# Performance work log

Hardware: AMD Instinct MI355X
Metric: run time of the kernel (lower is better)

## Reference

```python
import jax, jax.numpy as jnp
import numpy as np

N, E, NG = 8192, 65536, 8
EMB, SH = 32, 9
HID = EMB * SH
SDIM, M, KV = 16, 2048, 16  # M = master_rate*N masters (static top-k); KV virtual nbrs/node
RMAX, NB, PC = 10.0, 8, 5
MLPD, MSH, NL = 64, 32, 3
NEMB = 10


def _radial(r):
    # r: [E,1] -> Bessel basis * polynomial cutoff envelope, [E, NB]
    x = r / RMAX
    n = jnp.arange(1, NB + 1, dtype=r.dtype)
    bes = jnp.sqrt(2.0 / RMAX) * jnp.sin(n * jnp.pi * x) / jnp.maximum(r, 1e-9)
    p = float(PC)
    env = (1.0 - (p + 1) * (p + 2) / 2 * x ** PC + p * (p + 2) * x ** (PC + 1)
           - p * (p + 1) / 2 * x ** (PC + 2))
    env = jnp.where(x < 1.0, env, 0.0)
    return bes * env


def _sph(vec):
    # component-normalized real spherical harmonics l=0,1,2 of normalized vec
    r = jnp.linalg.norm(vec, axis=-1, keepdims=True)
    u = vec / jnp.maximum(r, 1e-9)
    x, y, z = u[..., 0], u[..., 1], u[..., 2]
    s3, s5, s15 = jnp.sqrt(3.0), jnp.sqrt(5.0), jnp.sqrt(15.0)
    Y = jnp.stack([
        jnp.ones_like(x),
        s3 * y, s3 * z, s3 * x,
        s15 * x * y, s15 * y * z, 0.5 * s5 * (3 * z * z - 1.0),
        s15 * x * z, 0.5 * s15 * (x * x - y * y)], axis=-1)
    return Y, r


def _conv(h, src, dst, sh, ef, W, rw1, rb1, rw2, rb2, valid, nnodes):
    # TFN-style conv: per-edge radial MLP -> per-sh-path weights, tensor product, scatter-sum
    rad = jax.nn.relu(ef @ rw1 + rb1) @ rw2 + rb2  # [E, SH]
    coeff = sh * rad                               # [E, SH]
    h_src = h[src]                                 # gather [E, in]
    out = W.shape[-1]
    msg = jnp.zeros((src.shape[0], out), h.dtype)
    for s in range(SH):  # small fixed loop over sh paths (avoids [E,in*SH] blowup)
        msg = msg + coeff[:, s:s + 1] * (h_src @ W[:, s, :])
    if valid is not None:
        msg = msg * valid[:, None]
    return jnp.zeros((nnodes, out), h.dtype).at[dst].add(msg)


def _scatter_softmax(sc, idx, nseg):
    mx = jax.ops.segment_max(sc, idx, nseg)
    e = jnp.exp(sc - mx[idx])
    s = jax.ops.segment_sum(e, idx, nseg)
    return e / (s[idx] + 1e-9)


def _forward(atoms, pos, edge_index, batch_ids, emb_table, W0, W12,
             rw1, rb1, rw2, rb2, msw1, msb1, msw2, msb2,
             vq, vk, aw1, ab1, aw2, ab2, pw1, pb1, pw2, pb2):
    h = emb_table[atoms]
    src, dst = edge_index[0], edge_index[1]
    for i in range(NL):
        W = W0 if i == 0 else W12[i - 1]
        # ---- local message passing over original edges ----
        vec = pos[src] - pos[dst]
        sh, r = _sph(vec)
        ef = _radial(r)
        h_up = _conv(h, src, dst, sh, ef, W, rw1[i], rb1[i], rw2[i], rb2[i], None, N)
        h_local = h_up.at[:, :h.shape[-1]].add(h)  # h_update + right-pad(h)
        # ---- master selection (static top-k of soft scores, k = master_rate*N) ----
        hs = h_local[:, :SDIM]
        m = jax.nn.sigmoid((jax.nn.relu(hs @ msw1[i] + msb1[i]) @ msw2[i] + msb2[i])[:, 0])
        _, midx = jax.lax.top_k(m, M)
        midx = jnp.sort(midx)
        inv = jnp.full((N,), -1, jnp.int32).at[midx].set(jnp.arange(M, dtype=jnp.int32))
        ms, md = inv[src], inv[dst]
        vi = (ms >= 0) & (md >= 0)           # induced-subgraph edge mask
        msc = jnp.where(vi, ms, 0)
        mdc = jnp.where(vi, md, 0)
        vif = vi.astype(h.dtype)
        h_m = h_local[midx]
        pos_m = pos[midx]
        hms = h_m[:, :SDIM]
        # induced dense adjacency over masters
        adj = jnp.minimum(jnp.zeros((M, M), h.dtype).at[msc, mdc].add(vif), 1.0)
        # ---- virtual edge generation (attention over masters) ----
        S = (hms @ vq[i]) @ (hms @ vk[i]).T / jnp.sqrt(jnp.asarray(SDIM, h.dtype))
        blocked = jnp.eye(M, dtype=bool) | (adj > 0)
        S = jnp.where(blocked, -jnp.inf, S)
        A_virtual = jax.nn.softmax(S, axis=-1)
        _, tk = jax.lax.top_k(S, KV)          # top-KV virtual nbrs per master (static)
        row = jnp.repeat(jnp.arange(M), KV)
        col = tk.reshape(-1)
        sv = jnp.concatenate([row, col])      # undirected virtual edges
        dv = jnp.concatenate([col, row])
        # ---- master-level edges: induced (masked) + virtual ----
        srcm = jnp.concatenate([msc, sv])
        dstm = jnp.concatenate([mdc, dv])
        vecm = pos_m[srcm] - pos_m[dstm]
        shm, rm = _sph(vecm)
        efm = _radial(rm)
        # scatter-softmax attention weights on virtual edges
        att_in = jnp.concatenate([hms[sv], hms[dv], efm[E:]], axis=-1)
        sc = (jax.nn.relu(att_in @ aw1[i] + ab1[i]) @ aw2[i] + ab2[i])[:, 0]
        wv = _scatter_softmax(sc, dv, M)
        full_w = jnp.concatenate([vif, wv])   # induced edges weight 1 (0 if invalid)
        efm = efm * full_w[:, None]
        if i == 0:
            h_hier = h_m  # first layer: in_irreps != out_irreps -> skip master conv
        else:
            validm = jnp.concatenate([vif, jnp.ones_like(wv)])
            h_mu = _conv(h_m, srcm, dstm, shm, efm, W,
                         rw1[i], rb1[i], rw2[i], rb2[i], validm, M)
            h_hier = h_mu + h_m
        # ---- scatter masters back, soft mix ----
        h_exp = jnp.zeros_like(h_local).at[midx].set(h_hier)
        me = m[:, None]
        h = (1.0 - me) * h_local + me * h_exp
    pooled = jax.ops.segment_sum(h[:, :EMB], batch_ids, NG)  # global_add_pool
    return jax.nn.relu(pooled @ pw1 + pb1) @ pw2 + pb2


def setup_inputs() -> dict:
    key = jax.random.key(0)
    ks = jax.random.split(key, 30)
    g = lambda k, shape, s=0.1: jax.random.normal(k, shape, jnp.float32) * s
    return dict(
        atoms=jax.random.randint(ks[0], (N,), 0, NEMB),
        pos=jax.random.normal(ks[1], (N, 3), jnp.float32) * 3.0,
        edge_index=jax.random.randint(ks[2], (2, E), 0, N),
        batch_ids=jnp.sort(jax.random.randint(ks[3], (N,), 0, NG)),
        emb_table=g(ks[4], (NEMB, EMB), 1.0),
        W0=g(ks[5], (EMB, SH, HID)),
        W12=g(ks[6], (NL - 1, HID, SH, HID), 0.05),
        rw1=g(ks[7], (NL, NB, MLPD), 0.3), rb1=g(ks[8], (NL, MLPD)),
        rw2=g(ks[9], (NL, MLPD, SH), 0.3), rb2=g(ks[10], (NL, SH)),
        msw1=g(ks[11], (NL, SDIM, MSH), 0.3), msb1=g(ks[12], (NL, MSH)),
        msw2=g(ks[13], (NL, MSH, 1), 0.3), msb2=g(ks[14], (NL, 1)),
        vq=g(ks[15], (NL, SDIM, SDIM), 0.3), vk=g(ks[16], (NL, SDIM, SDIM), 0.3),
        aw1=g(ks[17], (NL, 2 * SDIM + NB, SDIM), 0.3), ab1=g(ks[18], (NL, SDIM)),
        aw2=g(ks[19], (NL, SDIM, 1), 0.3), ab2=g(ks[20], (NL, 1)),
        pw1=g(ks[21], (EMB, EMB), 0.3), pb1=g(ks[22], (EMB,)),
        pw2=g(ks[23], (EMB, 1), 0.3), pb2=g(ks[24], (1,)),
    )


def reference(atoms, pos, edge_index, batch_ids, emb_table, W0, W12,
              rw1, rb1, rw2, rb2, msw1, msb1, msw2, msb2,
              vq, vk, aw1, ab1, aw2, ab2, pw1, pb1, pw2, pb2):
    return _forward(atoms, pos, edge_index, batch_ids, emb_table, W0, W12,
                    rw1, rb1, rw2, rb2, msw1, msb1, msw2, msb2,
                    vq, vk, aw1, ab1, aw2, ab2, pw1, pb1, pw2, pb2)
```

## Files before the change

### kernel.cpp

```cpp
#include <hip/hip_runtime.h>
#include <math.h>

#define NN     8192
#define EE     65536
#define NGR    8
#define EMBD   32
#define NSH    9
#define HIDD   288
#define SD     16
#define MM     2048
#define KVK    16
#define NBAS   8
#define MLPDIM 64
#define MSHD   32
#define MK     (MM*KVK)
#define EH     (EE + 2*MK)

static __device__ __forceinline__ float relu_(float x) { return fmaxf(x, 0.f); }

__device__ __forceinline__ void radial8(float r, float ef[8]) {
  float x = r * 0.1f;
  float invr = 1.0f / fmaxf(r, 1e-9f);
  float env = 0.0f;
  if (x < 1.0f) {
    float x2 = x * x, x4 = x2 * x2, x5 = x4 * x;
    env = 1.0f - 21.0f * x5 + 35.0f * x5 * x - 15.0f * x5 * x2;
  }
  const float cst = 0.4472135954999579f;
  float a = 3.14159265358979323846f * x;
#pragma unroll
  for (int n = 1; n <= NBAS; ++n)
    ef[n - 1] = cst * sinf((float)n * a) * invr * env;
}

__device__ __forceinline__ void sph9(float vx, float vy, float vz, float Y[9], float& r) {
  r = sqrtf(vx * vx + vy * vy + vz * vz);
  float inv = 1.0f / fmaxf(r, 1e-9f);
  float x = vx * inv, y = vy * inv, z = vz * inv;
  const float s3 = 1.7320508075688772f, s5 = 2.23606797749979f, s15 = 3.872983346207417f;
  Y[0] = 1.0f;
  Y[1] = s3 * y; Y[2] = s3 * z; Y[3] = s3 * x;
  Y[4] = s15 * x * y; Y[5] = s15 * y * z;
  Y[6] = 0.5f * s5 * (3.0f * z * z - 1.0f);
  Y[7] = s15 * x * z;
  Y[8] = 0.5f * s15 * (x * x - y * y);
}

__device__ __forceinline__ void radmlp(const float ef[8], const float* w1, const float* b1,
                                       const float* w2, const float* b2, float rad[9]) {
  float z[MLPDIM];
#pragma unroll
  for (int d = 0; d < MLPDIM; ++d) {
    float a = b1[d];
#pragma unroll
    for (int b = 0; b < NBAS; ++b) a += ef[b] * w1[b * MLPDIM + d];
    z[d] = relu_(a);
  }
#pragma unroll
  for (int s = 0; s < 9; ++s) {
    float a = b2[s];
#pragma unroll
    for (int d = 0; d < MLPDIM; ++d) a += z[d] * w2[d * 9 + s];
    rad[s] = a;
  }
}

__device__ __forceinline__ unsigned int fkey(float f) {
  unsigned int u = __float_as_uint(f);
  return (u & 0x80000000u) ? ~u : (u | 0x80000000u);
}
__device__ __forceinline__ float funkey(unsigned int k) {
  unsigned int u = (k & 0x80000000u) ? (k ^ 0x80000000u) : ~k;
  return __uint_as_float(u);
}

__device__ __forceinline__ void svdv(int j, const int* __restrict__ tkb, int& s, int& d) {
  if (j < MK) { s = j / KVK; d = tkb[j]; }
  else        { int t = j - MK; s = tkb[t]; d = t / KVK; }
}
__device__ __forceinline__ int dvof(int j, const int* __restrict__ tkb) {
  return (j < MK) ? tkb[j] : (j - MK) / KVK;
}


__global__ void k_init_h(const int* __restrict__ atoms, const float* __restrict__ emb,
                         float* __restrict__ hA) {
  int t = blockIdx.x * 256 + threadIdx.x;
  int n = t / HIDD, c = t - n * HIDD;
  hA[t] = (c < EMBD) ? emb[atoms[n] * EMBD + c] : 0.0f;
}

__global__ void k_geom(const float* __restrict__ pos, const int* __restrict__ ei,
                       float* __restrict__ sh_e, float* __restrict__ ef_e) {
  int e = blockIdx.x * 256 + threadIdx.x;
  int s = ei[e], d = ei[EE + e];
  float vx = pos[s * 3] - pos[d * 3];
  float vy = pos[s * 3 + 1] - pos[d * 3 + 1];
  float vz = pos[s * 3 + 2] - pos[d * 3 + 2];
  float Y[9], r;
  sph9(vx, vy, vz, Y, r);
  float ef[8]; radial8(r, ef);
#pragma unroll
  for (int t = 0; t < 9; ++t) sh_e[e * 9 + t] = Y[t];
#pragma unroll
  for (int b = 0; b < 8; ++b) ef_e[e * 8 + b] = ef[b];
}

__global__ __launch_bounds__(256) void k_radcoeff(const float* __restrict__ ef_e,
    const float* __restrict__ sh_e, const float* __restrict__ rw1, const float* __restrict__ rb1,
    const float* __restrict__ rw2, const float* __restrict__ rb2, float* __restrict__ coeff) {
  __shared__ float w1[NBAS * MLPDIM], b1[MLPDIM], w2[MLPDIM * 9], b2[9];
  int tid = threadIdx.x;
  for (int t = tid; t < NBAS * MLPDIM; t += 256) w1[t] = rw1[t];
  for (int t = tid; t < MLPDIM * 9; t += 256) w2[t] = rw2[t];
  if (tid < MLPDIM) b1[tid] = rb1[tid];
  if (tid < 9) b2[tid] = rb2[tid];
  __syncthreads();
  int e = blockIdx.x * 256 + tid;
  float ef[8];
#pragma unroll
  for (int b = 0; b < 8; ++b) ef[b] = ef_e[e * 8 + b];
  float rad[9]; radmlp(ef, w1, b1, w2, b2, rad);
#pragma unroll
  for (int s = 0; s < 9; ++s) coeff[(size_t)e * 9 + s] = sh_e[e * 9 + s] * rad[s];
}

__global__ void k_hist(const int* __restrict__ didx, int n, int* __restrict__ cnt) {
  int e = blockIdx.x * 256 + threadIdx.x;
  if (e >= n) return;
  int d = didx[e];
  if (d >= 0) atomicAdd(&cnt[d], 1);
}
__global__ __launch_bounds__(256) void k_scan(const int* __restrict__ cnt, int* __restrict__ off,
                                              int* __restrict__ cur, int nb) {
  __shared__ int ps[257];
  int tid = threadIdx.x;
  int chunk = nb / 256;
  int s = 0;
  for (int i = 0; i < chunk; ++i) s += cnt[tid * chunk + i];
  __shared__ int part[256];
  part[tid] = s;
  __syncthreads();
  if (tid == 0) {
    int a = 0;
    for (int i = 0; i < 256; ++i) { ps[i] = a; a += part[i]; }
    ps[256] = a;
  }
  __syncthreads();
  int a = ps[tid];
  for (int i = 0; i < chunk; ++i) {
    int idx = tid * chunk + i;
    off[idx] = a; cur[idx] = a;
    a += cnt[idx];
  }
  if (tid == 255) off[nb] = a;
}
__global__ void k_scat(const int* __restrict__ didx, int n, int* __restrict__ cur,
                       int* __restrict__ elist) {
  int e = blockIdx.x * 256 + threadIdx.x;
  if (e >= n) return;
  int d = didx[e];
  if (d < 0) return;
  int pos = atomicAdd(&cur[d], 1);
  elist[pos] = e;
}

template <int NJ, int Q>
__global__ __launch_bounds__(256) void k_gatherB(const float* __restrict__ h,
    const float* __restrict__ coeff, const int* __restrict__ sidx,
    const int* __restrict__ elist, const int* __restrict__ off, float* __restrict__ G) {
  constexpr int INW = (NJ == 1) ? 32 : 288;
  constexpr int KG = INW * 9;
  constexpr int NW = 4 * Q;
  __shared__ float red[3][64][NJ * 9];
  int w = threadIdx.x >> 6, l = threadIdx.x & 63;
  int d = blockIdx.x, q = blockIdx.y;
  int e0 = off[d], e1 = off[d + 1];
  float acc[NJ][9];
#pragma unroll
  for (int j = 0; j < NJ; ++j)
#pragma unroll
    for (int s = 0; s < 9; ++s) acc[j][s] = 0.f;
  for (int p = e0 + q * 4 + w; p < e1; p += NW) {
    int e = elist[p];
    int src = sidx[e];
    const float* hr = h + (size_t)src * HIDD;
    float hv[NJ];
#pragma unroll
    for (int j = 0; j < NJ; ++j)
      hv[j] = (l + 64 * j < INW) ? hr[l + 64 * j] : 0.f;
    const float* cfp = coeff + (size_t)e * 9;
    float cf[9];
#pragma unroll
    for (int s = 0; s < 9; ++s) cf[s] = cfp[s];
#pragma unroll
    for (int j = 0; j < NJ; ++j)
#pragma unroll
      for (int s = 0; s < 9; ++s) acc[j][s] += hv[j] * cf[s];
  }
  if (w > 0) {
#pragma unroll
    for (int j = 0; j < NJ; ++j)
#pragma unroll
      for (int s = 0; s < 9; ++s) red[w - 1][l][j * 9 + s] = acc[j][s];
  }
  __syncthreads();
  if (w == 0) {
    float* Gd = G + ((size_t)q * gridDim.x + d) * KG;
#pragma unroll
    for (int j = 0; j < NJ; ++j) {
      int k = l + 64 * j;
      if (k < INW) {
#pragma unroll
        for (int s = 0; s < 9; ++s) {
          float v = acc[j][s] + red[0][l][j * 9 + s] + red[1][l][j * 9 + s] +
                    red[2][l][j * 9 + s];
          Gd[k * 9 + s] = v;
        }
      }
    }
  }
}

template <int KK, int Q>
__global__ __launch_bounds__(256) void k_gemm64(const float* __restrict__ A,
    const float* __restrict__ B, float* __restrict__ Cpart) {
  constexpr int ktiles = KK / 16;
  __shared__ float As[16][68];
  __shared__ float Bs[16][192];
  int m0 = blockIdx.x * 64, cb = blockIdx.y * 144;
  int M = gridDim.x * 64;
  size_t Astride = (size_t)M * KK;
  int Z = gridDim.z, z = blockIdx.z;
  int t0 = (z * ktiles) / Z, t1 = ((z + 1) * ktiles) / Z;
  float* C = Cpart + (size_t)z * M * 288;
  int tid = threadIdx.x;
  int tx = tid & 15, ty = tid >> 4;
  int ar = tid & 63, ak = (tid >> 6) * 4;
  int bkb = tid >> 4, bcg = tid & 15;
  float acc[4][9];
#pragma unroll
  for (int i = 0; i < 4; ++i)
#pragma unroll
    for (int j = 0; j < 9; ++j) acc[i][j] = 0.f;
  for (int kt = t0; kt < t1; ++kt) {
    int k0 = kt * 16;
    size_t abase = (size_t)(m0 + ar) * KK + k0 + ak;
    float4 av = *(const float4*)&A[abase];
    if constexpr (Q > 1) {
#pragma unroll
      for (int qq = 1; qq < Q; ++qq) {
        float4 t = *(const float4*)&A[qq * Astride + abase];
        av.x += t.x; av.y += t.y; av.z += t.z; av.w += t.w;
      }
    }
    float bst[9];
#pragma unroll
    for (int u = 0; u < 9; ++u)
      bst[u] = B[(size_t)(k0 + bkb) * 288 + cb + bcg * 9 + u];
    __syncthreads();
    As[ak + 0][ar] = av.x; As[ak + 1][ar] = av.y;
    As[ak + 2][ar] = av.z; As[ak + 3][ar] = av.w;
#pragma unroll
    for (int u = 0; u < 9; ++u) Bs[bkb][bcg * 12 + u] = bst[u];
    __syncthreads();
#pragma unroll
    for (int k = 0; k < 16; ++k) {
      float4 a4 = *(const float4*)&As[k][4 * tx];
      float4 y0 = *(const float4*)&Bs[k][12 * ty];
      float4 y1 = *(const float4*)&Bs[k][12 * ty + 4];
      float y2 = Bs[k][12 * ty + 8];
      float b[9] = {y0.x, y0.y, y0.z, y0.w, y1.x, y1.y, y1.z, y1.w, y2};
#pragma unroll
      for (int j = 0; j < 9; ++j) {
        acc[0][j] += a4.x * b[j]; acc[1][j] += a4.y * b[j];
        acc[2][j] += a4.z * b[j]; acc[3][j] += a4.w * b[j];
      }
    }
    __syncthreads();
  }
#pragma unroll
  for (int i = 0; i < 4; ++i) {
    size_t rbase = (size_t)(m0 + 4 * tx + i) * 288 + cb + 9 * ty;
#pragma unroll
    for (int j = 0; j < 9; ++j) C[rbase + j] = acc[i][j];
  }
}

template <int Z>
__global__ void k_redN(const float* __restrict__ part, const float* __restrict__ hA,
                       float* __restrict__ hB, int INL) {
  int t = blockIdx.x * 256 + threadIdx.x;
  float v = 0.f;
#pragma unroll
  for (int z = 0; z < Z; ++z) v += part[(size_t)z * NN * 288 + t];
  int c = t % 288;
  if (c < INL) v += hA[t];
  hB[t] = v;
}
template <int Z>
__global__ void k_redH(const float* __restrict__ part, const float* __restrict__ hM,
                       float* __restrict__ hMu) {
  int t = blockIdx.x * 256 + threadIdx.x;
  float v = hM[t];
#pragma unroll
  for (int z = 0; z < Z; ++z) v += part[(size_t)z * MM * 288 + t];
  hMu[t] = v;
}

__global__ __launch_bounds__(256) void k_mmlp(const float* __restrict__ hB,
    const float* __restrict__ msw1, const float* __restrict__ msb1,
    const float* __restrict__ msw2, const float* __restrict__ msb2, float* __restrict__ mbuf) {
  __shared__ float w1[SD * MSHD], b1[MSHD], w2[MSHD];
  __shared__ float b2s;
  int tid = threadIdx.x;
  for (int t = tid; t < SD * MSHD; t += 256) w1[t] = msw1[t];
  if (tid < MSHD) { b1[tid] = msb1[tid]; w2[tid] = msw2[tid]; }
  if (tid == 0) b2s = msb2[0];
  __syncthreads();
  int n = blockIdx.x * 256 + tid;
  float hs[SD];
#pragma unroll
  for (int k = 0; k < SD; ++k) hs[k] = hB[(size_t)n * HIDD + k];
  float acc = b2s;
#pragma unroll
  for (int d = 0; d < MSHD; ++d) {
    float a = b1[d];
#pragma unroll
    for (int k = 0; k < SD; ++k) a += hs[k] * w1[k * MSHD + d];
    acc += relu_(a) * w2[d];
  }
  mbuf[n] = 1.0f / (1.0f + expf(-acc));
}

__global__ __launch_bounds__(256) void k_rank2(const float* __restrict__ mbuf,
                                               int* __restrict__ rankb) {
  __shared__ float vj[1024];
  __shared__ float vi_s[64];
  __shared__ int part[4][64];
  int tid = threadIdx.x;
  int i0 = blockIdx.x * 64, j0 = blockIdx.y * 1024;
  for (int t = tid; t < 1024; t += 256) vj[t] = mbuf[j0 + t];
  if (tid < 64) vi_s[tid] = mbuf[i0 + tid];
  __syncthreads();
  int il = tid & 63, js = tid >> 6;
  int i = i0 + il;
  float v = vi_s[il];
  int cnt = 0;
#pragma unroll 8
  for (int jj = js * 256; jj < js * 256 + 256; ++jj) {
    float w = vj[jj];
    cnt += (int)((w > v) | ((w == v) & (j0 + jj < i)));
  }
  part[js][il] = cnt;
  __syncthreads();
  if (tid < 64) {
    int c = part[0][tid] + part[1][tid] + part[2][tid] + part[3][tid];
    atomicAdd(&rankb[i0 + tid], c);
  }
}

__global__ __launch_bounds__(256) void k_select2(const int* __restrict__ rankb,
                                                 int* __restrict__ inv, int* __restrict__ midx) {
  __shared__ int part[256], ps[256];
  int tid = threadIdx.x;
  const int CH = NN / 256;
  int base = tid * CH;
  unsigned int mask = 0;
  int s = 0;
#pragma unroll
  for (int i = 0; i < CH; ++i) {
    int sel = (rankb[base + i] < MM) ? 1 : 0;
    mask |= (unsigned int)sel << i;
    s += sel;
  }
  part[tid] = s;
  __syncthreads();
  if (tid == 0) {
    int a = 0;
    for (int i = 0; i < 256; ++i) { ps[i] = a; a += part[i]; }
  }
  __syncthreads();
  int pos = ps[tid];
#pragma unroll
  for (int i = 0; i < CH; ++i) {
    if ((mask >> i) & 1u) {
      inv[base + i] = pos;
      midx[pos] = base + i;
      ++pos;
    } else {
      inv[base + i] = -1;
    }
  }
}

__global__ void k_gather_hm(const float* __restrict__ hB, const int* __restrict__ midx,
                            float* __restrict__ hM) {
  int t = blockIdx.x * 256 + threadIdx.x;
  int j = t / HIDD, c = t - j * HIDD;
  hM[t] = hB[(size_t)midx[j] * HIDD + c];
}

__global__ void k_gposm(const float* __restrict__ pos, const int* __restrict__ midx,
                        float* __restrict__ posm) {
  int j = blockIdx.x * 256 + threadIdx.x;
  int n = midx[j];
  posm[j * 3] = pos[n * 3];
  posm[j * 3 + 1] = pos[n * 3 + 1];
  posm[j * 3 + 2] = pos[n * 3 + 2];
}

__global__ void k_qk(const float* __restrict__ hM, const float* __restrict__ vq,
                     const float* __restrict__ vk, float* __restrict__ qb, float* __restrict__ kb) {
  int g = blockIdx.x * 256 + threadIdx.x;
  int j = g >> 5, c = g & 31;
  const float* w = (c < 16) ? vq : vk;
  int cc = c & 15;
  float a = 0.f;
#pragma unroll
  for (int k = 0; k < SD; ++k) a += hM[(size_t)j * HIDD + k] * w[k * SD + cc];
  if (c < 16) qb[j * SD + cc] = a; else kb[j * SD + cc] = a;
}

__global__ __launch_bounds__(256) void k_S(const float* __restrict__ qb,
                                           const float* __restrict__ kb, float* __restrict__ S) {
  __shared__ float qs[64][17], ks[64][17];
  int r0 = blockIdx.y * 64, c0 = blockIdx.x * 64;
  int tid = threadIdx.x;
  for (int t = tid; t < 64 * 16; t += 256) {
    qs[t / 16][t % 16] = qb[(size_t)(r0 + t / 16) * SD + t % 16];
    ks[t / 16][t % 16] = kb[(size_t)(c0 + t / 16) * SD + t % 16];
  }
  __syncthreads();
  int tx = tid & 15, ty = tid >> 4;
  float acc[4][4] = {};
#pragma unroll
  for (int k = 0; k < 16; ++k) {
    float a[4], b[4];
#pragma unroll
    for (int i = 0; i < 4; ++i) a[i] = qs[ty * 4 + i][k];
#pragma unroll
    for (int j = 0; j < 4; ++j) b[j] = ks[tx * 4 + j][k];
#pragma unroll
    for (int i = 0; i < 4; ++i)
#pragma unroll
      for (int j = 0; j < 4; ++j) acc[i][j] += a[i] * b[j];
  }
#pragma unroll
  for (int i = 0; i < 4; ++i)
#pragma unroll
    for (int j = 0; j < 4; ++j) {
      int r = r0 + ty * 4 + i, c = c0 + tx * 4 + j;
      S[(size_t)r * MM + c] = (r == c) ? -INFINITY : acc[i][j] * 0.25f;
    }
}

__global__ void k_adj(const int* __restrict__ ei, const int* __restrict__ inv,
                      float* __restrict__ S) {
  int e = blockIdx.x * 256 + threadIdx.x;
  int ms = inv[ei[e]], md = inv[ei[EE + e]];
  if (ms >= 0 && md >= 0) S[(size_t)ms * MM + md] = -INFINITY;
}

__global__ __launch_bounds__(64) void k_topkv(const float* __restrict__ S, int* __restrict__ tkb) {
  int row = blockIdx.x;
  int lane = threadIdx.x;
  const float* Sr = S + (size_t)row * MM;
  float v[32];
#pragma unroll
  for (int t = 0; t < 32; ++t) v[t] = Sr[lane + 64 * t];
  unsigned int selmask = 0;
  for (int it = 0; it < KVK; ++it) {
    float best = -INFINITY;
    int bcol = 0x7fffffff;
#pragma unroll
    for (int t = 0; t < 32; ++t) {
      if (!((selmask >> t) & 1u)) {
        int c = lane + 64 * t;
        float val = v[t];
        if (val > best || (val == best && c < bcol)) { best = val; bcol = c; }
      }
    }
#pragma unroll
    for (int off = 1; off < 64; off <<= 1) {
      float ov = __shfl_xor(best, off);
      int oc = __shfl_xor(bcol, off);
      if (ov > best || (ov == best && oc < bcol)) { best = ov; bcol = oc; }
    }
    if (lane == (bcol & 63)) selmask |= 1u << (bcol >> 6);
    if (lane == 0) tkb[row * KVK + it] = bcol;
  }
}

__global__ __launch_bounds__(256) void k_att(const float* __restrict__ hM,
    const float* __restrict__ posm, const int* __restrict__ tkb,
    const float* __restrict__ aw1, const float* __restrict__ ab1,
    const float* __restrict__ aw2, const float* __restrict__ ab2, float* __restrict__ scb) {
  __shared__ float w1[40 * SD], b1[SD], w2[SD];
  __shared__ float b2s;
  int tid = threadIdx.x;
  for (int t = tid; t < 40 * SD; t += 256) w1[t] = aw1[t];
  if (tid < SD) { b1[tid] = ab1[tid]; w2[tid] = aw2[tid]; }
  if (tid == 0) b2s = ab2[0];
  __syncthreads();
  int j = blockIdx.x * 256 + tid;
  int s, d; svdv(j, tkb, s, d);
  float vx = posm[s * 3] - posm[d * 3];
  float vy = posm[s * 3 + 1] - posm[d * 3 + 1];
  float vz = posm[s * 3 + 2] - posm[d * 3 + 2];
  float r = sqrtf(vx * vx + vy * vy + vz * vz);
  float ef[8]; radial8(r, ef);
  float hsv[SD], hdv[SD];
#pragma unroll
  for (int k = 0; k < SD; ++k) { hsv[k] = hM[(size_t)s * HIDD + k]; hdv[k] = hM[(size_t)d * HIDD + k]; }
  float acc = b2s;
#pragma unroll
  for (int o = 0; o < SD; ++o) {
    float a = b1[o];
#pragma unroll
    for (int k = 0; k < SD; ++k) a += hsv[k] * w1[k * SD + o];
#pragma unroll
    for (int k = 0; k < SD; ++k) a += hdv[k] * w1[(SD + k) * SD + o];
#pragma unroll
    for (int b = 0; b < 8; ++b) a += ef[b] * w1[(2 * SD + b) * SD + o];
    acc += relu_(a) * w2[o];
  }
  scb[j] = acc;
}

__global__ void k_segmax(const float* __restrict__ scb, const int* __restrict__ tkb,
                         unsigned int* __restrict__ segmax) {
  int j = blockIdx.x * 256 + threadIdx.x;
  atomicMax(&segmax[dvof(j, tkb)], fkey(scb[j]));
}
__global__ void k_segexp(const float* __restrict__ scb, const int* __restrict__ tkb,
                         const unsigned int* __restrict__ segmax, float* __restrict__ segsum,
                         float* __restrict__ wvb) {
  int j = blockIdx.x * 256 + threadIdx.x;
  int d = dvof(j, tkb);
  float e = expf(scb[j] - funkey(segmax[d]));
  wvb[j] = e;
  atomicAdd(&segsum[d], e);
}
__global__ void k_segnorm(const int* __restrict__ tkb, const float* __restrict__ segsum,
                          float* __restrict__ wvb) {
  int j = blockIdx.x * 256 + threadIdx.x;
  wvb[j] = wvb[j] / (segsum[dvof(j, tkb)] + 1e-9f);
}

__global__ void k_hier_first(const int* __restrict__ ei, const int* __restrict__ inv,
                             int* __restrict__ sb, int* __restrict__ db) {
  int e = blockIdx.x * 256 + threadIdx.x;
  int ms = inv[ei[e]], md = inv[ei[EE + e]];
  bool val = (ms >= 0) && (md >= 0);
  sb[e] = val ? ms : 0;
  db[e] = val ? md : -1;
}

__global__ __launch_bounds__(256) void k_coeff_virt(const float* __restrict__ posm,
    const int* __restrict__ tkb, const float* __restrict__ wvb,
    const float* __restrict__ rw1, const float* __restrict__ rb1,
    const float* __restrict__ rw2, const float* __restrict__ rb2,
    float* __restrict__ coeff, int* __restrict__ sb, int* __restrict__ db) {
  __shared__ float w1[NBAS * MLPDIM], b1[MLPDIM], w2[MLPDIM * 9], b2[9];
  int tid = threadIdx.x;
  for (int t = tid; t < NBAS * MLPDIM; t += 256) w1[t] = rw1[t];
  for (int t = tid; t < MLPDIM * 9; t += 256) w2[t] = rw2[t];
  if (tid < MLPDIM) b1[tid] = rb1[tid];
  if (tid < 9) b2[tid] = rb2[tid];
  __syncthreads();
  int j = blockIdx.x * 256 + tid;
  int s, d; svdv(j, tkb, s, d);
  float vx = posm[s * 3] - posm[d * 3];
  float vy = posm[s * 3 + 1] - posm[d * 3 + 1];
  float vz = posm[s * 3 + 2] - posm[d * 3 + 2];
  float Y[9], r;
  sph9(vx, vy, vz, Y, r);
  float ef[8]; radial8(r, ef);
  float w = wvb[j];
#pragma unroll
  for (int b = 0; b < 8; ++b) ef[b] *= w;
  float rad[9]; radmlp(ef, w1, b1, w2, b2, rad);
  int e = EE + j;
#pragma unroll
  for (int t = 0; t < 9; ++t) coeff[(size_t)e * 9 + t] = Y[t] * rad[t];
  sb[e] = s;
  db[e] = d;
}

__global__ void k_combine(const float* __restrict__ hB, const float* __restrict__ hier,
                          const float* __restrict__ mbuf, const int* __restrict__ inv,
                          float* __restrict__ hA) {
  int t = blockIdx.x * 256 + threadIdx.x;
  int n = t / HIDD;
  float f = mbuf[n];
  float v = (1.0f - f) * hB[t];
  int j = inv[n];
  if (j >= 0) v += f * hier[(size_t)j * HIDD + (t - n * HIDD)];
  hA[t] = v;
}

__global__ void k_pool(const float* __restrict__ hA, const int* __restrict__ bids,
                       float* __restrict__ pooled) {
  int t = blockIdx.x * 256 + threadIdx.x;
  int n = t / EMBD, c = t - n * EMBD;
  atomicAdd(&pooled[bids[n] * EMBD + c], hA[(size_t)n * HIDD + c]);
}

__global__ void k_head(const float* __restrict__ pooled, const float* __restrict__ pw1,
                       const float* __restrict__ pb1, const float* __restrict__ pw2,
                       const float* __restrict__ pb2, float* __restrict__ out) {
  __shared__ float z[NGR][EMBD];
  int tid = threadIdx.x;
  int g = tid / EMBD, c2 = tid % EMBD;
  if (g < NGR) {
    float a = pb1[c2];
    for (int c = 0; c < EMBD; ++c) a += pooled[g * EMBD + c] * pw1[c * EMBD + c2];
    z[g][c2] = relu_(a);
  }
  __syncthreads();
  if (tid < NGR) {
    float a = pb2[0];
    for (int c = 0; c < EMBD; ++c) a += z[tid][c] * pw2[c];
    out[tid] = a;
  }
}


extern "C" void kernel_launch(void* const* d_in, const int* in_sizes, int n_in,
                              void* d_out, int out_size, void* d_ws, size_t ws_size,
                              hipStream_t stream) {
  const int* atoms = (const int*)d_in[0];
  const float* pos = (const float*)d_in[1];
  const int* ei = (const int*)d_in[2];
  const int* bids = (const int*)d_in[3];
  const float* emb = (const float*)d_in[4];
  const float* W0 = (const float*)d_in[5];
  const float* W12 = (const float*)d_in[6];
  const float* rw1 = (const float*)d_in[7];
  const float* rb1 = (const float*)d_in[8];
  const float* rw2 = (const float*)d_in[9];
  const float* rb2 = (const float*)d_in[10];
  const float* msw1 = (const float*)d_in[11];
  const float* msb1 = (const float*)d_in[12];
  const float* msw2 = (const float*)d_in[13];
  const float* msb2 = (const float*)d_in[14];
  const float* vq = (const float*)d_in[15];
  const float* vk = (const float*)d_in[16];
  const float* aw1 = (const float*)d_in[17];
  const float* ab1 = (const float*)d_in[18];
  const float* aw2 = (const float*)d_in[19];
  const float* ab2 = (const float*)d_in[20];
  const float* pw1 = (const float*)d_in[21];
  const float* pb1 = (const float*)d_in[22];
  const float* pw2 = (const float*)d_in[23];
  const float* pb2 = (const float*)d_in[24];
  float* out = (float*)d_out;

  char* p = (char*)d_ws;
  auto alloc = [&](size_t n) { char* r = p; p += (n + 255) & ~(size_t)255; return r; };
  float* hA = (float*)alloc((size_t)NN * HIDD * 4);
  float* hB = (float*)alloc((size_t)NN * HIDD * 4);
  float* hM = (float*)alloc((size_t)MM * HIDD * 4);
  float* hMu = (float*)alloc((size_t)MM * HIDD * 4);
  float* S = (float*)alloc((size_t)MM * MM * 4);
  float* sh_e = (float*)alloc((size_t)EE * 9 * 4);
  float* ef_e = (float*)alloc((size_t)EE * 8 * 4);
  float* coeff = (float*)alloc((size_t)EH * 9 * 4);
  float* mbuf = (float*)alloc((size_t)NN * 4);
  int* rankb = (int*)alloc((size_t)NN * 4);
  int* inv = (int*)alloc((size_t)NN * 4);
  int* midx = (int*)alloc((size_t)MM * 4);
  float* posm = (float*)alloc((size_t)MM * 3 * 4);
  float* qb = (float*)alloc((size_t)MM * SD * 4);
  float* kb = (float*)alloc((size_t)MM * SD * 4);
  int* tkb = (int*)alloc((size_t)MM * KVK * 4);
  float* scb = (float*)alloc((size_t)2 * MK * 4);
  float* wvb = (float*)alloc((size_t)2 * MK * 4);
  unsigned int* segmax = (unsigned int*)alloc((size_t)MM * 4);
  float* segsum = (float*)alloc((size_t)MM * 4);
  int* sb = (int*)alloc((size_t)EH * 4);
  int* db = (int*)alloc((size_t)EH * 4);
  float* pooled = (float*)alloc((size_t)NGR * EMBD * 4);
  float* G = (float*)alloc((size_t)NN * 2592 * 4);
  float* Cpart = (float*)alloc((size_t)4 * NN * 288 * 4);
  int* cntN = (int*)alloc((size_t)NN * 4);
  int* offN = (int*)alloc((size_t)(NN + 1) * 4);
  int* curN = (int*)alloc((size_t)NN * 4);
  int* elN = (int*)alloc((size_t)EE * 4);
  int* cntH = (int*)alloc((size_t)MM * 4);
  int* offH = (int*)alloc((size_t)(MM + 1) * 4);
  int* curH = (int*)alloc((size_t)MM * 4);
  int* elH = (int*)alloc((size_t)EH * 4);

  const int* srcI = ei;
  const int* dstI = ei + EE;

  k_init_h<<<NN * HIDD / 256, 256, 0, stream>>>(atoms, emb, hA);
  k_geom<<<EE / 256, 256, 0, stream>>>(pos, ei, sh_e, ef_e);

  hipMemsetAsync(cntN, 0, NN * 4, stream);
  k_hist<<<EE / 256, 256, 0, stream>>>(dstI, EE, cntN);
  k_scan<<<1, 256, 0, stream>>>(cntN, offN, curN, NN);
  k_scat<<<EE / 256, 256, 0, stream>>>(dstI, EE, curN, elN);

  for (int L = 0; L < 3; ++L) {
    const float* W = (L == 0) ? W0 : (W12 + (size_t)(L - 1) * HIDD * 9 * HIDD);
    const float* lrw1 = rw1 + L * NBAS * MLPDIM;
    const float* lrb1 = rb1 + L * MLPDIM;
    const float* lrw2 = rw2 + L * MLPDIM * 9;
    const float* lrb2 = rb2 + L * 9;

    k_radcoeff<<<EE / 256, 256, 0, stream>>>(ef_e, sh_e, lrw1, lrb1, lrw2, lrb2, coeff);
    if (L == 0) {
      k_gatherB<1, 1><<<dim3(NN, 1), 256, 0, stream>>>(hA, coeff, srcI, elN, offN, G);
      k_gemm64<288, 1><<<dim3(NN / 64, 2, 2), 256, 0, stream>>>(G, W, Cpart);
      k_redN<2><<<NN * 288 / 256, 256, 0, stream>>>(Cpart, hA, hB, EMBD);
    } else {
      k_gatherB<5, 1><<<dim3(NN, 1), 256, 0, stream>>>(hA, coeff, srcI, elN, offN, G);
      k_gemm64<2592, 1><<<dim3(NN / 64, 2, 4), 256, 0, stream>>>(G, W, Cpart);
      k_redN<4><<<NN * 288 / 256, 256, 0, stream>>>(Cpart, hA, hB, HIDD);
    }
    k_mmlp<<<NN / 256, 256, 0, stream>>>(hB, msw1 + L * SD * MSHD, msb1 + L * MSHD,
                                         msw2 + L * MSHD, msb2 + L, mbuf);
    hipMemsetAsync(rankb, 0, NN * 4, stream);
    k_rank2<<<dim3(NN / 64, 8), 256, 0, stream>>>(mbuf, rankb);
    k_select2<<<1, 256, 0, stream>>>(rankb, inv, midx);
    k_gather_hm<<<MM * HIDD / 256, 256, 0, stream>>>(hB, midx, hM);

    if (L > 0) {
      k_gposm<<<MM / 256, 256, 0, stream>>>(pos, midx, posm);
      k_qk<<<MM * 32 / 256, 256, 0, stream>>>(hM, vq + L * SD * SD, vk + L * SD * SD, qb, kb);
      k_S<<<dim3(MM / 64, MM / 64), 256, 0, stream>>>(qb, kb, S);
      k_adj<<<EE / 256, 256, 0, stream>>>(ei, inv, S);
      k_topkv<<<MM, 64, 0, stream>>>(S, tkb);
      k_att<<<2 * MK / 256, 256, 0, stream>>>(hM, posm, tkb, aw1 + L * 40 * SD, ab1 + L * SD,
                                              aw2 + L * SD, ab2 + L, scb);
      hipMemsetAsync(segmax, 0, MM * 4, stream);
      hipMemsetAsync(segsum, 0, MM * 4, stream);
      k_segmax<<<2 * MK / 256, 256, 0, stream>>>(scb, tkb, segmax);
      k_segexp<<<2 * MK / 256, 256, 0, stream>>>(scb, tkb, segmax, segsum, wvb);
      k_segnorm<<<2 * MK / 256, 256, 0, stream>>>(tkb, segsum, wvb);
      k_hier_first<<<EE / 256, 256, 0, stream>>>(ei, inv, sb, db);
      k_coeff_virt<<<2 * MK / 256, 256, 0, stream>>>(posm, tkb, wvb, lrw1, lrb1, lrw2, lrb2,
                                                     coeff, sb, db);
      hipMemsetAsync(cntH, 0, MM * 4, stream);
      k_hist<<<EH / 256, 256, 0, stream>>>(db, EH, cntH);
      k_scan<<<1, 256, 0, stream>>>(cntH, offH, curH, MM);
      k_scat<<<EH / 256, 256, 0, stream>>>(db, EH, curH, elH);
      k_gatherB<5, 4><<<dim3(MM, 4), 256, 0, stream>>>(hM, coeff, sb, elH, offH, G);
      k_gemm64<2592, 4><<<dim3(MM / 64, 2, 8), 256, 0, stream>>>(G, W, Cpart);
      k_redH<8><<<MM * 288 / 256, 256, 0, stream>>>(Cpart, hM, hMu);
    }
    const float* hier = (L == 0) ? hM : hMu;
    k_combine<<<NN * HIDD / 256, 256, 0, stream>>>(hB, hier, mbuf, inv, hA);
  }

  hipMemsetAsync(pooled, 0, (size_t)NGR * EMBD * 4, stream);
  k_pool<<<NN * EMBD / 256, 256, 0, stream>>>(hA, bids, pooled);
  k_head<<<1, 256, 0, stream>>>(pooled, pw1, pb1, pw2, pb2, out);
}
```

Measured before the change: 1.483 ms.

## Enlarge GEMM tile to 128 rows and fold small gather/normalize kernels

The SGEMM kernel now uses 128-row tiles with an 8x9 per-thread register block, which halves B-tile reloads per output row and raises arithmetic intensity. Split-K factors are raised in places to keep enough blocks in flight, with the matching reduction kernels updated. The posm gather is merged into the hM gather kernel, and the softmax normalization is folded into k_coeff_virt, which removes two launches and one pass over wvb. The larger register tile may lower occupancy, and the extra split-K partials add reduction traffic.

```diff
diff --git a/kernel.cpp b/kernel.cpp
--- a/kernel.cpp
+++ b/kernel.cpp
@@ -223,35 +223,38 @@
 }
 
 template <int KK, int Q>
-__global__ __launch_bounds__(256) void k_gemm64(const float* __restrict__ A,
+__global__ __launch_bounds__(256) void k_gemm128(const float* __restrict__ A,
     const float* __restrict__ B, float* __restrict__ Cpart) {
   constexpr int ktiles = KK / 16;
-  __shared__ float As[16][68];
+  __shared__ float As[16][132];
   __shared__ float Bs[16][192];
-  int m0 = blockIdx.x * 64, cb = blockIdx.y * 144;
-  int M = gridDim.x * 64;
+  int m0 = blockIdx.x * 128, cb = blockIdx.y * 144;
+  int M = gridDim.x * 128;
   size_t Astride = (size_t)M * KK;
   int Z = gridDim.z, z = blockIdx.z;
   int t0 = (z * ktiles) / Z, t1 = ((z + 1) * ktiles) / Z;
   float* C = Cpart + (size_t)z * M * 288;
   int tid = threadIdx.x;
-  int tx = tid & 15, ty = tid >> 4;
-  int ar = tid & 63, ak = (tid >> 6) * 4;
+  int rowg = tid & 15, colg = tid >> 4;
+  int rA = tid >> 1, akofs = (tid & 1) * 8;
   int bkb = tid >> 4, bcg = tid & 15;
-  float acc[4][9];
-#pragma unroll
-  for (int i = 0; i < 4; ++i)
+  float acc[8][9];
+#pragma unroll
+  for (int i = 0; i < 8; ++i)
 #pragma unroll
     for (int j = 0; j < 9; ++j) acc[i][j] = 0.f;
   for (int kt = t0; kt < t1; ++kt) {
     int k0 = kt * 16;
-    size_t abase = (size_t)(m0 + ar) * KK + k0 + ak;
-    float4 av = *(const float4*)&A[abase];
+    size_t abase = (size_t)(m0 + rA) * KK + k0 + akofs;
+    float4 a0 = *(const float4*)&A[abase];
+    float4 a1 = *(const float4*)&A[abase + 4];
     if constexpr (Q > 1) {
 #pragma unroll
       for (int qq = 1; qq < Q; ++qq) {
-        float4 t = *(const float4*)&A[qq * Astride + abase];
-        av.x += t.x; av.y += t.y; av.z += t.z; av.w += t.w;
+        float4 t0v = *(const float4*)&A[qq * Astride + abase];
+        float4 t1v = *(const float4*)&A[qq * Astride + abase + 4];
+        a0.x += t0v.x; a0.y += t0v.y; a0.z += t0v.z; a0.w += t0v.w;
+        a1.x += t1v.x; a1.y += t1v.y; a1.z += t1v.z; a1.w += t1v.w;
       }
     }
     float bst[9];
@@ -259,29 +262,33 @@
     for (int u = 0; u < 9; ++u)
       bst[u] = B[(size_t)(k0 + bkb) * 288 + cb + bcg * 9 + u];
     __syncthreads();
-    As[ak + 0][ar] = av.x; As[ak + 1][ar] = av.y;
-    As[ak + 2][ar] = av.z; As[ak + 3][ar] = av.w;
+    As[akofs + 0][rA] = a0.x; As[akofs + 1][rA] = a0.y;
+    As[akofs + 2][rA] = a0.z; As[akofs + 3][rA] = a0.w;
+    As[akofs + 4][rA] = a1.x; As[akofs + 5][rA] = a1.y;
+    As[akofs + 6][rA] = a1.z; As[akofs + 7][rA] = a1.w;
 #pragma unroll
     for (int u = 0; u < 9; ++u) Bs[bkb][bcg * 12 + u] = bst[u];
     __syncthreads();
 #pragma unroll
     for (int k = 0; k < 16; ++k) {
-      float4 a4 = *(const float4*)&As[k][4 * tx];
-      float4 y0 = *(const float4*)&Bs[k][12 * ty];
-      float4 y1 = *(const float4*)&Bs[k][12 * ty + 4];
-      float y2 = Bs[k][12 * ty + 8];
+      float4 x0 = *(const float4*)&As[k][4 * rowg];
+      float4 x1 = *(const float4*)&As[k][64 + 4 * rowg];
+      float4 y0 = *(const float4*)&Bs[k][12 * colg];
+      float4 y1 = *(const float4*)&Bs[k][12 * colg + 4];
+      float y2 = Bs[k][12 * colg + 8];
+      float a[8] = {x0.x, x0.y, x0.z, x0.w, x1.x, x1.y, x1.z, x1.w};
       float b[9] = {y0.x, y0.y, y0.z, y0.w, y1.x, y1.y, y1.z, y1.w, y2};
 #pragma unroll
-      for (int j = 0; j < 9; ++j) {
-        acc[0][j] += a4.x * b[j]; acc[1][j] += a4.y * b[j];
-        acc[2][j] += a4.z * b[j]; acc[3][j] += a4.w * b[j];
-      }
+      for (int i = 0; i < 8; ++i)
+#pragma unroll
+        for (int j = 0; j < 9; ++j) acc[i][j] += a[i] * b[j];
     }
     __syncthreads();
   }
 #pragma unroll
-  for (int i = 0; i < 4; ++i) {
-    size_t rbase = (size_t)(m0 + 4 * tx + i) * 288 + cb + 9 * ty;
+  for (int i = 0; i < 8; ++i) {
+    int row = m0 + ((i < 4) ? (4 * rowg + i) : (64 + 4 * rowg + i - 4));
+    size_t rbase = (size_t)row * 288 + cb + 9 * colg;
 #pragma unroll
     for (int j = 0; j < 9; ++j) C[rbase + j] = acc[i][j];
   }
@@ -395,19 +402,13 @@
 }
 
 __global__ void k_gather_hm(const float* __restrict__ hB, const int* __restrict__ midx,
-                            float* __restrict__ hM) {
+                            const float* __restrict__ pos, float* __restrict__ hM,
+                            float* __restrict__ posm) {
   int t = blockIdx.x * 256 + threadIdx.x;
   int j = t / HIDD, c = t - j * HIDD;
-  hM[t] = hB[(size_t)midx[j] * HIDD + c];
-}
-
-__global__ void k_gposm(const float* __restrict__ pos, const int* __restrict__ midx,
-                        float* __restrict__ posm) {
-  int j = blockIdx.x * 256 + threadIdx.x;
   int n = midx[j];
-  posm[j * 3] = pos[n * 3];
-  posm[j * 3 + 1] = pos[n * 3 + 1];
-  posm[j * 3 + 2] = pos[n * 3 + 2];
+  hM[t] = hB[(size_t)n * HIDD + c];
+  if (c < 3) posm[j * 3 + c] = pos[n * 3 + c];
 }
 
 __global__ void k_qk(const float* __restrict__ hM, const float* __restrict__ vq,
@@ -542,11 +543,6 @@
   wvb[j] = e;
   atomicAdd(&segsum[d], e);
 }
-__global__ void k_segnorm(const int* __restrict__ tkb, const float* __restrict__ segsum,
-                          float* __restrict__ wvb) {
-  int j = blockIdx.x * 256 + threadIdx.x;
-  wvb[j] = wvb[j] / (segsum[dvof(j, tkb)] + 1e-9f);
-}
 
 __global__ void k_hier_first(const int* __restrict__ ei, const int* __restrict__ inv,
                              int* __restrict__ sb, int* __restrict__ db) {
@@ -559,6 +555,7 @@
 
 __global__ __launch_bounds__(256) void k_coeff_virt(const float* __restrict__ posm,
     const int* __restrict__ tkb, const float* __restrict__ wvb,
+    const float* __restrict__ segsum,
     const float* __restrict__ rw1, const float* __restrict__ rb1,
     const float* __restrict__ rw2, const float* __restrict__ rb2,
     float* __restrict__ coeff, int* __restrict__ sb, int* __restrict__ db) {
@@ -577,7 +574,7 @@
   float Y[9], r;
   sph9(vx, vy, vz, Y, r);
   float ef[8]; radial8(r, ef);
-  float w = wvb[j];
+  float w = wvb[j] / (segsum[d] + 1e-9f);
 #pragma unroll
   for (int b = 0; b < 8; ++b) ef[b] *= w;
   float rad[9]; radmlp(ef, w1, b1, w2, b2, rad);
@@ -714,11 +711,11 @@
     k_radcoeff<<<EE / 256, 256, 0, stream>>>(ef_e, sh_e, lrw1, lrb1, lrw2, lrb2, coeff);
     if (L == 0) {
       k_gatherB<1, 1><<<dim3(NN, 1), 256, 0, stream>>>(hA, coeff, srcI, elN, offN, G);
-      k_gemm64<288, 1><<<dim3(NN / 64, 2, 2), 256, 0, stream>>>(G, W, Cpart);
-      k_redN<2><<<NN * 288 / 256, 256, 0, stream>>>(Cpart, hA, hB, EMBD);
+      k_gemm128<288, 1><<<dim3(NN / 128, 2, 4), 256, 0, stream>>>(G, W, Cpart);
+      k_redN<4><<<NN * 288 / 256, 256, 0, stream>>>(Cpart, hA, hB, EMBD);
     } else {
       k_gatherB<5, 1><<<dim3(NN, 1), 256, 0, stream>>>(hA, coeff, srcI, elN, offN, G);
-      k_gemm64<2592, 1><<<dim3(NN / 64, 2, 4), 256, 0, stream>>>(G, W, Cpart);
+      k_gemm128<2592, 1><<<dim3(NN / 128, 2, 4), 256, 0, stream>>>(G, W, Cpart);
       k_redN<4><<<NN * 288 / 256, 256, 0, stream>>>(Cpart, hA, hB, HIDD);
     }
     k_mmlp<<<NN / 256, 256, 0, stream>>>(hB, msw1 + L * SD * MSHD, msb1 + L * MSHD,
@@ -726,10 +723,9 @@
     hipMemsetAsync(rankb, 0, NN * 4, stream);
     k_rank2<<<dim3(NN / 64, 8), 256, 0, stream>>>(mbuf, rankb);
     k_select2<<<1, 256, 0, stream>>>(rankb, inv, midx);
-    k_gather_hm<<<MM * HIDD / 256, 256, 0, stream>>>(hB, midx, hM);
+    k_gather_hm<<<MM * HIDD / 256, 256, 0, stream>>>(hB, midx, pos, hM, posm);
 
     if (L > 0) {
-      k_gposm<<<MM / 256, 256, 0, stream>>>(pos, midx, posm);
       k_qk<<<MM * 32 / 256, 256, 0, stream>>>(hM, vq + L * SD * SD, vk + L * SD * SD, qb, kb);
       k_S<<<dim3(MM / 64, MM / 64), 256, 0, stream>>>(qb, kb, S);
       k_adj<<<EE / 256, 256, 0, stream>>>(ei, inv, S);
@@ -740,17 +736,16 @@
       hipMemsetAsync(segsum, 0, MM * 4, stream);
       k_segmax<<<2 * MK / 256, 256, 0, stream>>>(scb, tkb, segmax);
       k_segexp<<<2 * MK / 256, 256, 0, stream>>>(scb, tkb, segmax, segsum, wvb);
-      k_segnorm<<<2 * MK / 256, 256, 0, stream>>>(tkb, segsum, wvb);
       k_hier_first<<<EE / 256, 256, 0, stream>>>(ei, inv, sb, db);
-      k_coeff_virt<<<2 * MK / 256, 256, 0, stream>>>(posm, tkb, wvb, lrw1, lrb1, lrw2, lrb2,
-                                                     coeff, sb, db);
+      k_coeff_virt<<<2 * MK / 256, 256, 0, stream>>>(posm, tkb, wvb, segsum,
+                                                     lrw1, lrb1, lrw2, lrb2, coeff, sb, db);
       hipMemsetAsync(cntH, 0, MM * 4, stream);
       k_hist<<<EH / 256, 256, 0, stream>>>(db, EH, cntH);
       k_scan<<<1, 256, 0, stream>>>(cntH, offH, curH, MM);
       k_scat<<<EH / 256, 256, 0, stream>>>(db, EH, curH, elH);
       k_gatherB<5, 4><<<dim3(MM, 4), 256, 0, stream>>>(hM, coeff, sb, elH, offH, G);
-      k_gemm64<2592, 4><<<dim3(MM / 64, 2, 8), 256, 0, stream>>>(G, W, Cpart);
-      k_redH<8><<<MM * 288 / 256, 256, 0, stream>>>(Cpart, hM, hMu);
+      k_gemm128<2592, 4><<<dim3(MM / 128, 2, 16), 256, 0, stream>>>(G, W, Cpart);
+      k_redH<16><<<MM * 288 / 256, 256, 0, stream>>>(Cpart, hM, hMu);
     }
     const float* hier = (L == 0) ? hM : hMu;
     k_combine<<<NN * HIDD / 256, 256, 0, stream>>>(hB, hier, mbuf, inv, hA);
```

Result: no change. 1.497 ms (+0.9%).
